# Performance work log

Measured on AMD Instinct MI355X. Metric: run time of the kernel, lower is better.

## Reference

```python
import jax, jax.numpy as jnp
import numpy as np

N_NODES = 50000
N_EDGES = 600000
D_IN = 128
D_OUT = 128
EPS = 1e-5


def setup_inputs() -> dict:
    key = jax.random.key(0)
    k1, k2, k3 = jax.random.split(key, 3)
    x = jax.random.normal(k1, (N_NODES, D_IN), dtype=jnp.float32)
    # GCNConv linear weight (bias=False), applied as x @ W.T
    W = jax.random.normal(k2, (D_OUT, D_IN), dtype=jnp.float32) * (1.0 / np.sqrt(D_IN))
    edge_index = jax.random.randint(k3, (2, N_EDGES), 0, N_NODES, dtype=jnp.int64)
    return {"x": x, "W": W, "edge_index": edge_index}


def reference(x, W, edge_index):
    N = x.shape[0]
    dtype = x.dtype
    # --- GCNConv: add self loops, symmetric normalization, gather-scatter ---
    loop = jnp.arange(N, dtype=edge_index.dtype)
    row = jnp.concatenate([edge_index[0], loop])  # source nodes
    col = jnp.concatenate([edge_index[1], loop])  # target nodes (aggregation)
    ew = jnp.ones(row.shape[0], dtype=dtype)
    deg = jax.ops.segment_sum(ew, col, num_segments=N)  # in-degree incl. self loops
    dinv = jnp.where(deg > 0, jax.lax.rsqrt(deg), 0.0)
    norm = dinv[row] * dinv[col]  # [E+N]
    xw = x @ W.T  # [N, D_OUT]
    msg = xw[row] * norm[:, None]  # gather + edge scaling
    out = jax.ops.segment_sum(msg, col, num_segments=N)  # scatter-add aggregation
    # --- PairNorm (scale=1.0, scale_individually=False) ---
    xc = out - out.mean(axis=0, keepdims=True)
    out = xc / jnp.sqrt(EPS + jnp.mean(jnp.sum(xc * xc, axis=-1)))
    # --- activation + residual ---
    return jax.nn.relu(out) + out
```

## Files before the change

### kernel.cpp

```cpp
#include <hip/hip_runtime.h>
#include <hip/hip_fp16.h>

#define EPS 1e-5f
#define NREP 16
#define REPSTRIDE 132
#define MAXDEG 48

typedef _Float16 half8_t __attribute__((ext_vector_type(8)));
typedef float floatx4 __attribute__((ext_vector_type(4)));

__global__ void scatter_kernel(const int* __restrict__ row, const int* __restrict__ col,
                               int* __restrict__ cursor, int* __restrict__ csr, int E) {
    int e = blockIdx.x * blockDim.x + threadIdx.x;
    if (e < E) {
        int c = col[e];
        int pos = atomicAdd(&cursor[c], 1);
        if (pos < MAXDEG) csr[c * MAXDEG + pos] = row[e];
    }
}

__global__ __launch_bounds__(256) void gemm_kernel(
    const float* __restrict__ x, const float* __restrict__ W,
    const int* __restrict__ cursor, __half* __restrict__ xsh, int N) {
    __shared__ _Float16 sw[128][136];

    int tid = threadIdx.x;
#pragma unroll
    for (int t = 0; t < 16; ++t) {
        int idx = tid + t * 256;
        int j = idx >> 5;
        int k4 = idx & 31;
        float4 v = ((const float4*)W)[idx];
        _Float16* d = &sw[j][k4 * 4];
        d[0] = (_Float16)v.x; d[1] = (_Float16)v.y;
        d[2] = (_Float16)v.z; d[3] = (_Float16)v.w;
    }
    __syncthreads();

    int w  = tid >> 6;
    int l  = tid & 63;
    int lr = l & 15;
    int kb = l >> 4;

    int rowA = blockIdx.x * 64 + w * 16 + lr;
    const float4* xr = (const float4*)&x[(size_t)min(rowA, N - 1) * 128];

    float4 xv[8];
#pragma unroll
    for (int kk = 0; kk < 4; ++kk) {
        xv[2 * kk]     = xr[8 * kk + 2 * kb];
        xv[2 * kk + 1] = xr[8 * kk + 2 * kb + 1];
    }
    half8_t a[4];
#pragma unroll
    for (int kk = 0; kk < 4; ++kk) {
        float4 v0 = xv[2 * kk], v1 = xv[2 * kk + 1];
        half8_t h;
        h[0] = (_Float16)v0.x; h[1] = (_Float16)v0.y;
        h[2] = (_Float16)v0.z; h[3] = (_Float16)v0.w;
        h[4] = (_Float16)v1.x; h[5] = (_Float16)v1.y;
        h[6] = (_Float16)v1.z; h[7] = (_Float16)v1.w;
        a[kk] = h;
    }

    floatx4 acc[8];
#pragma unroll
    for (int t = 0; t < 8; ++t) acc[t] = (floatx4){0.f, 0.f, 0.f, 0.f};

#pragma unroll
    for (int kk = 0; kk < 4; ++kk) {
#pragma unroll
        for (int t = 0; t < 8; ++t) {
            half8_t b = *(const half8_t*)&sw[16 * t + lr][32 * kk + 8 * kb];
            acc[t] = __builtin_amdgcn_mfma_f32_16x16x32_f16(a[kk], b, acc[t], 0, 0, 0);
        }
    }

    int rbase = blockIdx.x * 64 + w * 16 + 4 * kb;
    float dv[4];
#pragma unroll
    for (int r = 0; r < 4; ++r)
        dv[r] = (rbase + r < N) ? rsqrtf((float)(cursor[rbase + r] + 1)) : 0.f;
#pragma unroll
    for (int r = 0; r < 4; ++r) {
        int grow = rbase + r;
        if (grow < N) {
#pragma unroll
            for (int t = 0; t < 8; ++t)
                xsh[(size_t)grow * 128 + 16 * t + lr] = __float2half(acc[t][r] * dv[r]);
        }
    }
}

__global__ void gather_kernel(const __half2* __restrict__ xs2, const int* __restrict__ cursor,
                              const int* __restrict__ csr,
                              float* __restrict__ pre, float* __restrict__ colrep,
                              float* __restrict__ ssrep, int N) {
    __shared__ float scol[128];
    __shared__ float sss;
    if (threadIdx.x < 128) scol[threadIdx.x] = 0.f;
    if (threadIdx.x == 0) sss = 0.f;
    __syncthreads();

    int lane = threadIdx.x & 63;
    int wid = (blockIdx.x * blockDim.x + threadIdx.x) >> 6;
    int nw  = (gridDim.x * blockDim.x) >> 6;
    float2* pre2 = (float2*)pre;
    float csx = 0.f, csy = 0.f, ss = 0.f;

    for (int n = wid; n < N; n += nw) {
        int deg = cursor[n];
        int e = min(deg, MAXDEG);
        const int* cs = &csr[n * MAXDEG];
        float2 acc = __half22float2(xs2[n * 64 + lane]);
        int p = 0;
        for (; p + 8 <= e; p += 8) {
            int idx[8];
#pragma unroll
            for (int t = 0; t < 8; ++t) idx[t] = cs[p + t];
            __half2 a[8];
#pragma unroll
            for (int t = 0; t < 8; ++t) a[t] = xs2[idx[t] * 64 + lane];
#pragma unroll
            for (int t = 0; t < 8; ++t) {
                float2 f = __half22float2(a[t]);
                acc.x += f.x; acc.y += f.y;
            }
        }
        if (p + 4 <= e) {
            int idx[4];
#pragma unroll
            for (int t = 0; t < 4; ++t) idx[t] = cs[p + t];
            __half2 a[4];
#pragma unroll
            for (int t = 0; t < 4; ++t) a[t] = xs2[idx[t] * 64 + lane];
#pragma unroll
            for (int t = 0; t < 4; ++t) {
                float2 f = __half22float2(a[t]);
                acc.x += f.x; acc.y += f.y;
            }
            p += 4;
        }
        for (; p < e; ++p) {
            float2 f = __half22float2(xs2[cs[p] * 64 + lane]);
            acc.x += f.x; acc.y += f.y;
        }
        float dv = rsqrtf((float)(deg + 1));
        float vx = acc.x * dv, vy = acc.y * dv;
        pre2[n * 64 + lane] = make_float2(vx, vy);
        csx += vx; csy += vy; ss += vx * vx + vy * vy;
    }

    atomicAdd(&scol[2 * lane], csx);
    atomicAdd(&scol[2 * lane + 1], csy);
    for (int d = 32; d > 0; d >>= 1) ss += __shfl_down(ss, d);
    if (lane == 0) atomicAdd(&sss, ss);
    __syncthreads();
    int rep = blockIdx.x & (NREP - 1);
    if (threadIdx.x < 128) atomicAdd(&colrep[rep * REPSTRIDE + threadIdx.x], scol[threadIdx.x]);
    if (threadIdx.x == 128) atomicAdd(&ssrep[rep], sss);
}

__global__ void final_kernel(float* __restrict__ out, const float* __restrict__ colrep,
                             const float* __restrict__ ssrep, int N, int total) {
    __shared__ float sm[128];
    __shared__ float red[128];
    __shared__ float sscale;
    int t = threadIdx.x;
    if (t < 128) {
        float cs = 0.f;
#pragma unroll
        for (int r = 0; r < NREP; ++r) cs += colrep[r * REPSTRIDE + t];
        float m = cs / (float)N;
        sm[t] = m;
        red[t] = m * m;
    }
    __syncthreads();
    for (int d = 64; d > 0; d >>= 1) {
        if (t < d) red[t] += red[t + d];
        __syncthreads();
    }
    if (t == 0) {
        float sq = 0.f;
#pragma unroll
        for (int r = 0; r < NREP; ++r) sq += ssrep[r];
        float tot = sq - (float)N * red[0];
        sscale = rsqrtf(EPS + tot / (float)N);
    }
    __syncthreads();
    float s = sscale;
    int tid = blockIdx.x * blockDim.x + threadIdx.x;
    int stride = gridDim.x * blockDim.x;
    for (int i = tid; i < total; i += stride) {
        float y = (out[i] - sm[i & 127]) * s;
        out[i] = y > 0.f ? 2.f * y : y;
    }
}

extern "C" void kernel_launch(void* const* d_in, const int* in_sizes, int n_in,
                              void* d_out, int out_size, void* d_ws, size_t ws_size,
                              hipStream_t stream) {
    const float* x = (const float*)d_in[0];
    const float* W = (const float*)d_in[1];
    const int* ei  = (const int*)d_in[2];
    int N = in_sizes[0] / 128;
    int E = in_sizes[2] / 2;
    const int* row = ei;
    const int* col = ei + E;
    float* out = (float*)d_out;

    __half* xsh      = (__half*)d_ws;
    int*   cursor    = (int*)((float*)d_ws + (size_t)N * 64);
    float* colrep    = (float*)(cursor + N);
    float* ssrep     = colrep + NREP * REPSTRIDE;
    int*   csr       = (int*)(ssrep + NREP);

    hipMemsetAsync(cursor, 0, (size_t)(N + NREP * REPSTRIDE + NREP) * 4, stream);

    scatter_kernel<<<(E + 255) / 256, 256, 0, stream>>>(row, col, cursor, csr, E);
    gemm_kernel   <<<(N + 63) / 64, 256, 0, stream>>>(x, W, cursor, xsh, N);
    gather_kernel <<<2048, 256, 0, stream>>>((const __half2*)xsh, cursor, csr,
                                             out, colrep, ssrep, N);
    final_kernel  <<<1024, 256, 0, stream>>>(out, colrep, ssrep, N, N * 128);
}
```

Baseline: 181.2 us.

## Split gather into four feature-slice passes with four nodes per wavefront

The gather kernel now runs four times. Each pass handles a 32-column slice of the features, and each wavefront processes four nodes at once with 16 lanes per node. The aim is a smaller gathered working set per pass so the randomly indexed rows fit better in cache, plus more independent loads in flight per wavefront. The pre-normalisation output is written with nontemporal stores. In exchange, CSR indices and degrees are reread four times, there are three extra kernel launches, and each gather touches only 64-byte segments.

```diff
diff --git a/kernel.cpp b/kernel.cpp
--- a/kernel.cpp
+++ b/kernel.cpp
@@ -8,6 +8,7 @@
 
 typedef _Float16 half8_t __attribute__((ext_vector_type(8)));
 typedef float floatx4 __attribute__((ext_vector_type(4)));
+typedef float floatx2 __attribute__((ext_vector_type(2)));
 
 __global__ void scatter_kernel(const int* __restrict__ row, const int* __restrict__ col,
                                int* __restrict__ cursor, int* __restrict__ csr, int E) {
@@ -95,7 +96,7 @@
 __global__ void gather_kernel(const __half2* __restrict__ xs2, const int* __restrict__ cursor,
                               const int* __restrict__ csr,
                               float* __restrict__ pre, float* __restrict__ colrep,
-                              float* __restrict__ ssrep, int N) {
+                              float* __restrict__ ssrep, int N, int pass) {
     __shared__ float scol[128];
     __shared__ float sss;
     if (threadIdx.x < 128) scol[threadIdx.x] = 0.f;
@@ -103,16 +104,27 @@
     __syncthreads();
 
     int lane = threadIdx.x & 63;
-    int wid = (blockIdx.x * blockDim.x + threadIdx.x) >> 6;
-    int nw  = (gridDim.x * blockDim.x) >> 6;
-    float2* pre2 = (float2*)pre;
+    int q = lane >> 4;
+    int c = lane & 15;
+    int s16 = pass * 16;
+    int wq = (blockIdx.x * blockDim.x + threadIdx.x) >> 6;
+    int nwq = (gridDim.x * blockDim.x) >> 6;
+    int Nq = (N + 3) >> 2;
+    floatx2* pre2 = (floatx2*)pre;
     float csx = 0.f, csy = 0.f, ss = 0.f;
 
-    for (int n = wid; n < N; n += nw) {
-        int deg = cursor[n];
-        int e = min(deg, MAXDEG);
-        const int* cs = &csr[n * MAXDEG];
-        float2 acc = __half22float2(xs2[n * 64 + lane]);
+    for (int nq = wq; nq < Nq; nq += nwq) {
+        int n = nq * 4 + q;
+        bool vn = n < N;
+        int nc = vn ? n : 0;
+        int deg = cursor[nc];
+        int e = vn ? min(deg, MAXDEG) : 0;
+        const int* cs = &csr[nc * MAXDEG];
+        float accx = 0.f, accy = 0.f;
+        if (vn) {
+            float2 f = __half22float2(xs2[nc * 64 + s16 + c]);
+            accx = f.x; accy = f.y;
+        }
         int p = 0;
         for (; p + 8 <= e; p += 8) {
             int idx[8];
@@ -120,11 +132,11 @@
             for (int t = 0; t < 8; ++t) idx[t] = cs[p + t];
             __half2 a[8];
 #pragma unroll
-            for (int t = 0; t < 8; ++t) a[t] = xs2[idx[t] * 64 + lane];
+            for (int t = 0; t < 8; ++t) a[t] = xs2[idx[t] * 64 + s16 + c];
 #pragma unroll
             for (int t = 0; t < 8; ++t) {
                 float2 f = __half22float2(a[t]);
-                acc.x += f.x; acc.y += f.y;
+                accx += f.x; accy += f.y;
             }
         }
         if (p + 4 <= e) {
@@ -133,26 +145,29 @@
             for (int t = 0; t < 4; ++t) idx[t] = cs[p + t];
             __half2 a[4];
 #pragma unroll
-            for (int t = 0; t < 4; ++t) a[t] = xs2[idx[t] * 64 + lane];
+            for (int t = 0; t < 4; ++t) a[t] = xs2[idx[t] * 64 + s16 + c];
 #pragma unroll
             for (int t = 0; t < 4; ++t) {
                 float2 f = __half22float2(a[t]);
-                acc.x += f.x; acc.y += f.y;
+                accx += f.x; accy += f.y;
             }
             p += 4;
         }
         for (; p < e; ++p) {
-            float2 f = __half22float2(xs2[cs[p] * 64 + lane]);
-            acc.x += f.x; acc.y += f.y;
-        }
-        float dv = rsqrtf((float)(deg + 1));
-        float vx = acc.x * dv, vy = acc.y * dv;
-        pre2[n * 64 + lane] = make_float2(vx, vy);
+            float2 f = __half22float2(xs2[cs[p] * 64 + s16 + c]);
+            accx += f.x; accy += f.y;
+        }
+        float dv = vn ? rsqrtf((float)(deg + 1)) : 0.f;
+        float vx = accx * dv, vy = accy * dv;
+        if (vn) {
+            floatx2 st; st[0] = vx; st[1] = vy;
+            __builtin_nontemporal_store(st, &pre2[(size_t)n * 64 + s16 + c]);
+        }
         csx += vx; csy += vy; ss += vx * vx + vy * vy;
     }
 
-    atomicAdd(&scol[2 * lane], csx);
-    atomicAdd(&scol[2 * lane + 1], csy);
+    atomicAdd(&scol[2 * (s16 + c)], csx);
+    atomicAdd(&scol[2 * (s16 + c) + 1], csy);
     for (int d = 32; d > 0; d >>= 1) ss += __shfl_down(ss, d);
     if (lane == 0) atomicAdd(&sss, ss);
     __syncthreads();
@@ -219,7 +234,8 @@
 
     scatter_kernel<<<(E + 255) / 256, 256, 0, stream>>>(row, col, cursor, csr, E);
     gemm_kernel   <<<(N + 63) / 64, 256, 0, stream>>>(x, W, cursor, xsh, N);
-    gather_kernel <<<2048, 256, 0, stream>>>((const __half2*)xsh, cursor, csr,
-                                             out, colrep, ssrep, N);
+    for (int pass = 0; pass < 4; ++pass)
+        gather_kernel <<<2048, 256, 0, stream>>>((const __half2*)xsh, cursor, csr,
+                                                 out, colrep, ssrep, N, pass);
     final_kernel  <<<1024, 256, 0, stream>>>(out, colrep, ssrep, N, N * 128);
 }
```

Result: slower. 281.8 us (+55.6%).
